# Optimization experiments

Hardware: AMD Instinct MI355X
Metric: run time of the kernel (lower is better)

## Reference

```python
import jax, jax.numpy as jnp
from jax import lax
import numpy as np

T = 3          # num_frame
DIV = 2        # channel_shift div
PAD = 1        # kernel_size//2 (same padding for k=3)


def setup_inputs() -> dict:
    key = jax.random.key(0)
    k1, k2 = jax.random.split(key)
    x = jax.random.normal(k1, (12, 64, 256, 256), dtype=jnp.float32)      # (B*T, C, H, W)
    weight = jax.random.normal(k2, (64, 64, 3, 3), dtype=jnp.float32)     # (O, I, kh, kw)
    return {"x": x, "weight": weight}


def reference(x, weight):
    BT, C, H, W = x.shape
    B = BT // T
    # channel_shift: view (B, T*C, H, W), roll by C//div along channel axis
    shift = C // DIV
    y = x.reshape(B, T * C, H, W)
    y = jnp.roll(y, shift, axis=1).reshape(BT, C, H, W)
    # BinaryConv2d: sign(activations), sign(weights) * per-out-channel mean|W|
    scale = jnp.mean(jnp.abs(weight), axis=(1, 2, 3), keepdims=True)      # (O,1,1,1)
    bw = jnp.sign(weight) * scale
    bx = jnp.sign(y)
    out = lax.conv_general_dilated(
        bx, bw,
        window_strides=(1, 1),
        padding=[(PAD, PAD), (PAD, PAD)],
        dimension_numbers=("NCHW", "OIHW", "NCHW"),
    )
    return out
```

## Files before the change

kernel.cpp:

```cpp
#include <hip/hip_runtime.h>
#include <stdint.h>

typedef unsigned long long u64;
typedef unsigned int u32;

#define HW 65536
#define WD 256

__global__ __launch_bounds__(64) void pack_w_kernel(const float* __restrict__ wt,
                                                    u64* __restrict__ pw,
                                                    float* __restrict__ scale) {
    const int o = blockIdx.x;
    const int i = threadIdx.x;
    const float* p = wt + o * 576 + i * 9;
    float v[9];
    float s = 0.f;
#pragma unroll
    for (int k = 0; k < 9; k++) { v[k] = p[k]; s += fabsf(v[k]); }
#pragma unroll
    for (int k = 0; k < 9; k++) {
        u64 m = __ballot((__float_as_uint(v[k]) >> 31) != 0u);
        if (i == 0) pw[o * 9 + k] = m;
    }
#pragma unroll
    for (int off = 32; off > 0; off >>= 1) s += __shfl_down(s, off);
    if (i == 0) scale[o] = s * (1.0f / 576.0f);
}

#define LROWS 10
#define LCOLS 72
#define NGRP  18

__global__ __launch_bounds__(256) void fused_kernel(const float* __restrict__ x,
                                                    const u64* __restrict__ pw,
                                                    const float* __restrict__ scale,
                                                    float* __restrict__ out) {
    const int tx = blockIdx.x;
    const int ty = blockIdx.y;
    const int n  = blockIdx.z;
    const int gw0 = tx << 6;
    const int gh0 = ty << 3;

    const int b = n / 3;
    const int t = n - b * 3;
    const int fp = b * 3 + (t + 2) % 3;

    const float* xa = x + ((size_t)fp * 64 + 32) * HW;
    const float* xb = x + (size_t)n * 64 * HW;

    __shared__ u64 ph[LROWS][LCOLS];

    const int tid = threadIdx.x;

    if (tid < LROWS * NGRP) {
        const int row = tid / NGRP;
        const int grp = tid - row * NGRP;
        const int gh  = gh0 - 1 + row;
        const int gwb = gw0 - 4 + (grp << 2);
        u64 w0 = 0, w1 = 0, w2 = 0, w3 = 0;
        if ((gh >= 0) & (gh < 256) & (gwb >= 0) & (gwb < 256)) {
            const float* pa = xa + (size_t)gh * WD + gwb;
            const float* pb = xb + (size_t)gh * WD + gwb;
            u32 l0 = 0, l1 = 0, l2 = 0, l3 = 0;
            u32 h0 = 0, h1 = 0, h2 = 0, h3 = 0;
#pragma unroll
            for (int c = 0; c < 32; c++) {
                float4 va = *(const float4*)(pa + (size_t)c * HW);
                l0 |= (__float_as_uint(va.x) >> 31) << c;
                l1 |= (__float_as_uint(va.y) >> 31) << c;
                l2 |= (__float_as_uint(va.z) >> 31) << c;
                l3 |= (__float_as_uint(va.w) >> 31) << c;
                float4 vb = *(const float4*)(pb + (size_t)c * HW);
                h0 |= (__float_as_uint(vb.x) >> 31) << c;
                h1 |= (__float_as_uint(vb.y) >> 31) << c;
                h2 |= (__float_as_uint(vb.z) >> 31) << c;
                h3 |= (__float_as_uint(vb.w) >> 31) << c;
            }
            w0 = ((u64)h0 << 32) | l0;
            w1 = ((u64)h1 << 32) | l1;
            w2 = ((u64)h2 << 32) | l2;
            w3 = ((u64)h3 << 32) | l3;
        }
        const int c0 = grp << 2;
        ph[row][c0 + 0] = w0;
        ph[row][c0 + 1] = w1;
        ph[row][c0 + 2] = w2;
        ph[row][c0 + 3] = w3;
    }
    __syncthreads();

    const int q  = tid >> 6;
    const int w  = tid & 63;
    const int gw = gw0 + w;
    const bool edge_block = (tx == 0) | (tx == 3) | (ty == 0) | (ty == 31);

    float* op = out + (size_t)n * 64 * HW + gw;

#pragma unroll
    for (int k = 0; k < 2; k++) {
        const int hl = q + (k << 2);
        const int gh = gh0 + hl;
        u64 xv[9];
#pragma unroll
        for (int dr = 0; dr < 3; dr++)
#pragma unroll
            for (int dc = 0; dc < 3; dc++)
                xv[dr * 3 + dc] = ph[hl + dr][w + 3 + dc];

        float* oprow = op + (size_t)gh * WD;

        if (!edge_block) {
#pragma unroll 4
            for (int o = 0; o < 64; o++) {
                const u64* wp = pw + o * 9;
                int cnt = 0;
#pragma unroll
                for (int kk = 0; kk < 9; kk++) cnt += __popcll(xv[kk] ^ wp[kk]);
                const float sc = scale[o];
                __builtin_nontemporal_store(fmaf(-2.f * sc, (float)cnt, 576.f * sc),
                                            oprow + (size_t)o * HW);
            }
        } else {
            u64 mk[9];
            int ninv = 0;
#pragma unroll
            for (int dr = -1; dr <= 1; dr++) {
#pragma unroll
                for (int dc = -1; dc <= 1; dc++) {
                    const int hh = gh + dr, ww = gw + dc;
                    const bool valid = (hh >= 0) && (hh < 256) && (ww >= 0) && (ww < 256);
                    mk[(dr + 1) * 3 + (dc + 1)] = valid ? ~0ull : 0ull;
                    ninv += valid ? 0 : 1;
                }
            }
            const int basecnt = 32 * ninv;

#pragma unroll 4
            for (int o = 0; o < 64; o++) {
                const u64* wp = pw + o * 9;
                int cnt = basecnt;
#pragma unroll
                for (int kk = 0; kk < 9; kk++) cnt += __popcll((xv[kk] ^ wp[kk]) & mk[kk]);
                const float sc = scale[o];
                __builtin_nontemporal_store(fmaf(-2.f * sc, (float)cnt, 576.f * sc),
                                            oprow + (size_t)o * HW);
            }
        }
    }
}

extern "C" void kernel_launch(void* const* d_in, const int* in_sizes, int n_in,
                              void* d_out, int out_size, void* d_ws, size_t ws_size,
                              hipStream_t stream) {
    (void)in_sizes; (void)n_in; (void)out_size; (void)ws_size;
    const float* x  = (const float*)d_in[0];
    const float* wt = (const float*)d_in[1];
    float* out = (float*)d_out;

    u64* pw = (u64*)d_ws;
    float* scale = (float*)(pw + 576);

    pack_w_kernel<<<64, 64, 0, stream>>>(wt, pw, scale);
    fused_kernel<<<dim3(4, 32, 12), 256, 0, stream>>>(x, pw, scale, out);
}
```

Baseline: 374.9 us.

## Use full-width 2-row tiles with 4 outputs per thread and precomputed border corrections

After: 374.8 us. Within noise of the previous version (-0.0%).

```diff
diff --git a/kernel.cpp b/kernel.cpp
--- a/kernel.cpp
+++ b/kernel.cpp
@@ -3,43 +3,60 @@
 
 typedef unsigned long long u64;
 typedef unsigned int u32;
+typedef float fx4 __attribute__((ext_vector_type(4)));
 
 #define HW 65536
 #define WD 256
 
 __global__ __launch_bounds__(64) void pack_w_kernel(const float* __restrict__ wt,
                                                     u64* __restrict__ pw,
-                                                    float* __restrict__ scale) {
+                                                    float* __restrict__ scale,
+                                                    u32* __restrict__ aux) {
     const int o = blockIdx.x;
     const int i = threadIdx.x;
     const float* p = wt + o * 576 + i * 9;
     float v[9];
+    u64 mm[9];
     float s = 0.f;
 #pragma unroll
     for (int k = 0; k < 9; k++) { v[k] = p[k]; s += fabsf(v[k]); }
 #pragma unroll
     for (int k = 0; k < 9; k++) {
-        u64 m = __ballot((__float_as_uint(v[k]) >> 31) != 0u);
-        if (i == 0) pw[o * 9 + k] = m;
+        mm[k] = __ballot((__float_as_uint(v[k]) >> 31) != 0u);
+        if (i == 0) pw[o * 9 + k] = mm[k];
     }
 #pragma unroll
     for (int off = 32; off > 0; off >>= 1) s += __shfl_down(s, off);
-    if (i == 0) scale[o] = s * (1.0f / 576.0f);
+    if (i == 0) {
+        scale[o] = s * (1.0f / 576.0f);
+        int pc[9];
+#pragma unroll
+        for (int k = 0; k < 9; k++) pc[k] = 32 - (int)__popcll(mm[k]);
+        u32* a = aux + o * 8;
+        a[0] = pc[0] + pc[3] + pc[6];
+        a[1] = pc[3] + pc[6];
+        a[2] = pc[0] + pc[3];
+        a[3] = pc[2] + pc[5] + pc[8];
+        a[4] = pc[5] + pc[8];
+        a[5] = pc[2] + pc[5];
+        a[6] = pc[0] + pc[1] + pc[2];
+        a[7] = pc[6] + pc[7] + pc[8];
+    }
 }
 
-#define LROWS 10
-#define LCOLS 72
-#define NGRP  18
+#define LSTRIDE 260
 
 __global__ __launch_bounds__(256) void fused_kernel(const float* __restrict__ x,
                                                     const u64* __restrict__ pw,
                                                     const float* __restrict__ scale,
+                                                    const u32* __restrict__ aux,
                                                     float* __restrict__ out) {
-    const int tx = blockIdx.x;
-    const int ty = blockIdx.y;
-    const int n  = blockIdx.z;
-    const int gw0 = tx << 6;
-    const int gh0 = ty << 3;
+    __shared__ u64 ph[4][LSTRIDE];
+
+    const int bx = blockIdx.x;
+    const int n  = blockIdx.y;
+    const int ty = ((bx & 7) << 4) | (bx >> 3);
+    const int gh0 = ty << 1;
 
     const int b = n / 3;
     const int t = n - b * 3;
@@ -48,19 +65,15 @@
     const float* xa = x + ((size_t)fp * 64 + 32) * HW;
     const float* xb = x + (size_t)n * 64 * HW;
 
-    __shared__ u64 ph[LROWS][LCOLS];
+    const int lane = threadIdx.x & 63;
+    const int wv   = threadIdx.x >> 6;
 
-    const int tid = threadIdx.x;
-
-    if (tid < LROWS * NGRP) {
-        const int row = tid / NGRP;
-        const int grp = tid - row * NGRP;
-        const int gh  = gh0 - 1 + row;
-        const int gwb = gw0 - 4 + (grp << 2);
-        u64 w0 = 0, w1 = 0, w2 = 0, w3 = 0;
-        if ((gh >= 0) & (gh < 256) & (gwb >= 0) & (gwb < 256)) {
-            const float* pa = xa + (size_t)gh * WD + gwb;
-            const float* pb = xb + (size_t)gh * WD + gwb;
+    {
+        const int gh = gh0 - 1 + wv;
+        u64* dst = ph[wv];
+        if ((gh >= 0) & (gh < 256)) {
+            const float* pa = xa + (size_t)gh * WD + (lane << 2);
+            const float* pb = xb + (size_t)gh * WD + (lane << 2);
             u32 l0 = 0, l1 = 0, l2 = 0, l3 = 0;
             u32 h0 = 0, h1 = 0, h2 = 0, h3 = 0;
 #pragma unroll
@@ -76,76 +89,79 @@
                 h2 |= (__float_as_uint(vb.z) >> 31) << c;
                 h3 |= (__float_as_uint(vb.w) >> 31) << c;
             }
-            w0 = ((u64)h0 << 32) | l0;
-            w1 = ((u64)h1 << 32) | l1;
-            w2 = ((u64)h2 << 32) | l2;
-            w3 = ((u64)h3 << 32) | l3;
+            const int c0i = 1 + (lane << 2);
+            dst[c0i + 0] = ((u64)h0 << 32) | l0;
+            dst[c0i + 1] = ((u64)h1 << 32) | l1;
+            dst[c0i + 2] = ((u64)h2 << 32) | l2;
+            dst[c0i + 3] = ((u64)h3 << 32) | l3;
+            if (lane == 0)  dst[0]   = 0;
+            if (lane == 63) dst[257] = 0;
+        } else {
+#pragma unroll
+            for (int j = 0; j < 4; j++) dst[lane + (j << 6)] = 0;
+            if (lane < 2) dst[256 + lane] = 0;
         }
-        const int c0 = grp << 2;
-        ph[row][c0 + 0] = w0;
-        ph[row][c0 + 1] = w1;
-        ph[row][c0 + 2] = w2;
-        ph[row][c0 + 3] = w3;
     }
     __syncthreads();
 
-    const int q  = tid >> 6;
-    const int w  = tid & 63;
-    const int gw = gw0 + w;
-    const bool edge_block = (tx == 0) | (tx == 3) | (ty == 0) | (ty == 31);
+    const int rloc  = wv & 1;
+    const int obase = (wv >> 1) << 5;
+    const int gh    = gh0 + rloc;
+    const bool vtop = (gh > 0);
+    const bool vbot = (gh < 255);
+    const bool inner = vtop & vbot;
+    const int lci = vtop ? (vbot ? 0 : 2) : 1;
+    const int rci = lci + 3;
+    const int bci = vtop ? 7 : 6;
+    const bool lane0 = (lane == 0), lane63 = (lane == 63);
 
-    float* op = out + (size_t)n * 64 * HW + gw;
+    const u64* r0p = &ph[rloc    ][lane << 2];
+    const u64* r1p = &ph[rloc + 1][lane << 2];
+    const u64* r2p = &ph[rloc + 2][lane << 2];
+    const u64 tL = r0p[0], tA = r0p[1], tB = r0p[2], tC = r0p[3], tD = r0p[4], tR = r0p[5];
+    const u64 mL = r1p[0], mA = r1p[1], mB = r1p[2], mC = r1p[3], mD = r1p[4], mR = r1p[5];
+    const u64 bL = r2p[0], bA = r2p[1], bB = r2p[2], bC = r2p[3], bD = r2p[4], bR = r2p[5];
 
-#pragma unroll
-    for (int k = 0; k < 2; k++) {
-        const int hl = q + (k << 2);
-        const int gh = gh0 + hl;
-        u64 xv[9];
-#pragma unroll
-        for (int dr = 0; dr < 3; dr++)
-#pragma unroll
-            for (int dc = 0; dc < 3; dc++)
-                xv[dr * 3 + dc] = ph[hl + dr][w + 3 + dc];
+    float* op = out + (size_t)n * 64 * HW + (size_t)gh * WD + (lane << 2);
 
-        float* oprow = op + (size_t)gh * WD;
+#pragma unroll 2
+    for (int oi = 0; oi < 32; oi++) {
+        const int o = obase + oi;
+        const u64* wp = pw + o * 9;
+        const u64 w0 = wp[0], w1 = wp[1], w2 = wp[2];
+        const u64 w3 = wp[3], w4 = wp[4], w5 = wp[5];
+        const u64 w6 = wp[6], w7 = wp[7], w8 = wp[8];
+        const u32* ao = aux + (o << 3);
+        const int bc  = inner ? 0 : (int)ao[bci];
+        const int lcv = (int)ao[lci], rcv = (int)ao[rci];
 
-        if (!edge_block) {
-#pragma unroll 4
-            for (int o = 0; o < 64; o++) {
-                const u64* wp = pw + o * 9;
-                int cnt = 0;
-#pragma unroll
-                for (int kk = 0; kk < 9; kk++) cnt += __popcll(xv[kk] ^ wp[kk]);
-                const float sc = scale[o];
-                __builtin_nontemporal_store(fmaf(-2.f * sc, (float)cnt, 576.f * sc),
-                                            oprow + (size_t)o * HW);
-            }
-        } else {
-            u64 mk[9];
-            int ninv = 0;
-#pragma unroll
-            for (int dr = -1; dr <= 1; dr++) {
-#pragma unroll
-                for (int dc = -1; dc <= 1; dc++) {
-                    const int hh = gh + dr, ww = gw + dc;
-                    const bool valid = (hh >= 0) && (hh < 256) && (ww >= 0) && (ww < 256);
-                    mk[(dr + 1) * 3 + (dc + 1)] = valid ? ~0ull : 0ull;
-                    ninv += valid ? 0 : 1;
-                }
-            }
-            const int basecnt = 32 * ninv;
+        int c0 = bc + (lane0  ? lcv : 0);
+        int c1 = bc, c2 = bc;
+        int c3 = bc + (lane63 ? rcv : 0);
 
-#pragma unroll 4
-            for (int o = 0; o < 64; o++) {
-                const u64* wp = pw + o * 9;
-                int cnt = basecnt;
-#pragma unroll
-                for (int kk = 0; kk < 9; kk++) cnt += __popcll((xv[kk] ^ wp[kk]) & mk[kk]);
-                const float sc = scale[o];
-                __builtin_nontemporal_store(fmaf(-2.f * sc, (float)cnt, 576.f * sc),
-                                            oprow + (size_t)o * HW);
-            }
-        }
+        c0 += __popcll(tL ^ w0) + __popcll(tA ^ w1) + __popcll(tB ^ w2);
+        c1 += __popcll(tA ^ w0) + __popcll(tB ^ w1) + __popcll(tC ^ w2);
+        c2 += __popcll(tB ^ w0) + __popcll(tC ^ w1) + __popcll(tD ^ w2);
+        c3 += __popcll(tC ^ w0) + __popcll(tD ^ w1) + __popcll(tR ^ w2);
+
+        c0 += __popcll(mL ^ w3) + __popcll(mA ^ w4) + __popcll(mB ^ w5);
+        c1 += __popcll(mA ^ w3) + __popcll(mB ^ w4) + __popcll(mC ^ w5);
+        c2 += __popcll(mB ^ w3) + __popcll(mC ^ w4) + __popcll(mD ^ w5);
+        c3 += __popcll(mC ^ w3) + __popcll(mD ^ w4) + __popcll(mR ^ w5);
+
+        c0 += __popcll(bL ^ w6) + __popcll(bA ^ w7) + __popcll(bB ^ w8);
+        c1 += __popcll(bA ^ w6) + __popcll(bB ^ w7) + __popcll(bC ^ w8);
+        c2 += __popcll(bB ^ w6) + __popcll(bC ^ w7) + __popcll(bD ^ w8);
+        c3 += __popcll(bC ^ w6) + __popcll(bD ^ w7) + __popcll(bR ^ w8);
+
+        const float sc = scale[o];
+        const float fa = -2.f * sc, fb = 576.f * sc;
+        fx4 v;
+        v.x = fmaf(fa, (float)c0, fb);
+        v.y = fmaf(fa, (float)c1, fb);
+        v.z = fmaf(fa, (float)c2, fb);
+        v.w = fmaf(fa, (float)c3, fb);
+        __builtin_nontemporal_store(v, (fx4*)(op + (size_t)o * HW));
     }
 }
 
@@ -159,7 +175,8 @@
 
     u64* pw = (u64*)d_ws;
     float* scale = (float*)(pw + 576);
+    u32* aux = (u32*)(scale + 64);
 
-    pack_w_kernel<<<64, 64, 0, stream>>>(wt, pw, scale);
-    fused_kernel<<<dim3(4, 32, 12), 256, 0, stream>>>(x, pw, scale, out);
+    pack_w_kernel<<<64, 64, 0, stream>>>(wt, pw, scale, aux);
+    fused_kernel<<<dim3(128, 12), 256, 0, stream>>>(x, pw, scale, aux, out);
 }
```
